# Kernel tuning notes

Measured on AMD Instinct MI355X. Metric: run time of the kernel, lower is better.

Reference implementation:

```python
import jax, jax.numpy as jnp
import numpy as np

S, B, D, H, E, K, DF = 1024, 16, 512, 8, 16, 2, 2048
HD = D // H
EPS = 1e-5


def _layernorm(x, g, b):
    m = x.mean(-1, keepdims=True)
    v = ((x - m) ** 2).mean(-1, keepdims=True)
    return (x - m) / jnp.sqrt(v + EPS) * g + b


def setup_inputs() -> dict:
    key = jax.random.key(0)
    ks = jax.random.split(key, 10)
    s = 0.02
    return {
        "src": jax.random.normal(ks[0], (S, B, D), jnp.float32),
        "pos": jax.random.normal(ks[1], (S, B, D), jnp.float32),
        "in_proj_w": jax.random.normal(ks[2], (3 * D, D), jnp.float32) * s,
        "in_proj_b": jnp.zeros((3 * D,), jnp.float32),
        "out_w": jax.random.normal(ks[3], (D, D), jnp.float32) * s,
        "out_b": jnp.zeros((D,), jnp.float32),
        "norm1_g": jnp.ones((D,), jnp.float32),
        "norm1_b": jnp.zeros((D,), jnp.float32),
        "gate_w": jax.random.normal(ks[4], (E, D), jnp.float32) * s,
        "gate_b": jnp.zeros((E,), jnp.float32),
        "w1": jax.random.normal(ks[5], (E, DF, D), jnp.float32) * s,
        "b1": jnp.zeros((E, DF), jnp.float32),
        "w2": jax.random.normal(ks[6], (E, D, DF), jnp.float32) * s,
        "b2": jnp.zeros((E, D), jnp.float32),
    }


def reference(src, pos, in_proj_w, in_proj_b, out_w, out_b, norm1_g, norm1_b,
              gate_w, gate_b, w1, b1, w2, b2):
    # ---- self attention (torch nn.MultiheadAttention, seq-first) ----
    qk_in = src + pos                      # q = k = src + pos, v = src
    wq, wk, wv = jnp.split(in_proj_w, 3, axis=0)
    bq, bk, bv = jnp.split(in_proj_b, 3, axis=0)
    q = qk_in @ wq.T + bq                  # [S,B,D]
    k = qk_in @ wk.T + bk
    v = src @ wv.T + bv

    def heads(x):                          # [S,B,D] -> [B,H,S,HD]
        return x.reshape(S, B, H, HD).transpose(1, 2, 0, 3)

    qh, kh, vh = heads(q), heads(k), heads(v)
    scores = jnp.einsum('bhqd,bhkd->bhqk', qh * (1.0 / np.sqrt(HD)), kh)
    attn = jax.nn.softmax(scores, axis=-1)
    o = jnp.einsum('bhqk,bhkd->bhqd', attn, vh)
    o = o.transpose(2, 0, 1, 3).reshape(S, B, D) @ out_w.T + out_b

    x = _layernorm(src + o, norm1_g, norm1_b)  # post-norm residual

    # ---- MoE FFN (FMoE NaiveGate, top-k=2, no capacity drop) ----
    t = x.reshape(S * B, D)                # tokens
    logits = t @ gate_w.T + gate_b         # [T,E]
    topv, topi = jax.lax.top_k(logits, K)  # [T,K]
    gate_score = jax.nn.softmax(topv, axis=-1)
    T = S * B
    comb = jnp.zeros((T, E), t.dtype).at[jnp.arange(T)[:, None], topi].add(gate_score)

    def body(acc, packed):
        W1, B1, W2, B2, c = packed         # per-expert weights + combine col [T]
        h = jax.nn.relu(t @ W1.T + B1)     # [T,DF]
        y = h @ W2.T + B2                  # [T,D]
        return acc + c[:, None] * y, None

    acc, _ = jax.lax.scan(body, jnp.zeros_like(t), (w1, b1, w2, b2, comb.T))
    # pre_lnorm=False branch: output = inp + core_out (internal LN unused)
    return x + acc.reshape(S, B, D)
```

## Files before the change

kernel.cpp:

```cpp
#include <hip/hip_runtime.h>
#include <hip/hip_bf16.h>

typedef float f4 __attribute__((ext_vector_type(4)));
typedef float f32x4 __attribute__((ext_vector_type(4)));
typedef short short8 __attribute__((ext_vector_type(8)));
typedef unsigned short u16x4 __attribute__((ext_vector_type(4)));
typedef unsigned short u16x8 __attribute__((ext_vector_type(8)));
typedef unsigned int u32x4 __attribute__((ext_vector_type(4)));
typedef unsigned int u32x8 __attribute__((ext_vector_type(8)));

#define S_LEN 1024
#define BATCH 16
#define DIM   512
#define NH    8
#define HDIM  64
#define NE    16
#define DFF   2048
#define T_TOK 16384
#define CAP   34816
#define BM    128

__device__ __forceinline__ unsigned short f2bf(float f) {
  union { float f; unsigned u; } v; v.f = f;
  unsigned r = v.u + 0x7fffu + ((v.u >> 16) & 1u);
  return (unsigned short)(r >> 16);
}
__device__ __forceinline__ float bf2f(unsigned short h) {
  union { unsigned u; float f; } v; v.u = ((unsigned)h) << 16;
  return v.f;
}

__device__ __forceinline__ void load_lds16(const void* g, void* l) {
  __builtin_amdgcn_global_load_lds(
      (__attribute__((address_space(1))) void*)(void*)g,
      (__attribute__((address_space(3))) void*)l, 16, 0, 0);
}

__device__ __forceinline__ short8 pack_hi8(const unsigned* val) {
  union { unsigned u[4]; short8 s; } t;
#pragma unroll
  for (int i = 0; i < 4; i++)
    t.u[i] = (val[2 * i] >> 16) | (val[2 * i + 1] & 0xFFFF0000u);
  return t.s;
}
__device__ __forceinline__ short8 pack_lo8(const unsigned* val) {
  union { unsigned u[4]; short8 s; } t;
#pragma unroll
  for (int i = 0; i < 4; i++)
    t.u[i] = (val[2 * i] & 0xFFFFu) | (val[2 * i + 1] << 16);
  return t.s;
}

__global__ __launch_bounds__(256) void k_cvt_bf16(const float* __restrict__ in,
                                                  unsigned short* __restrict__ outb,
                                                  size_t n) {
  size_t i = ((size_t)blockIdx.x * 256 + threadIdx.x) * 4;
  size_t stride = (size_t)gridDim.x * 1024;
  for (; i < n; i += stride) {
    f4 v = *(const f4*)&in[i];
    u16x4 o;
    o[0] = f2bf(v[0]); o[1] = f2bf(v[1]); o[2] = f2bf(v[2]); o[3] = f2bf(v[3]);
    *(u16x4*)&outb[i] = o;
  }
}

__global__ __launch_bounds__(256) void k_split_w(const float* __restrict__ in,
                                                 unsigned short* __restrict__ hi,
                                                 unsigned short* __restrict__ lo,
                                                 size_t n) {
  size_t i = ((size_t)blockIdx.x * 256 + threadIdx.x) * 4;
  size_t stride = (size_t)gridDim.x * 1024;
  for (; i < n; i += stride) {
    f4 v = *(const f4*)&in[i];
    u16x4 h, l;
#pragma unroll
    for (int j = 0; j < 4; j++) {
      unsigned short hh = f2bf(v[j]);
      h[j] = hh;
      l[j] = f2bf(v[j] - bf2f(hh));
    }
    *(u16x4*)&hi[i] = h;
    *(u16x4*)&lo[i] = l;
  }
}

__global__ __launch_bounds__(256) void k_init(int* __restrict__ slotTok,
                                              float* __restrict__ slotW,
                                              int* __restrict__ counts) {
  int i = blockIdx.x * 256 + threadIdx.x;
  if (i < CAP) { slotTok[i] = -1; slotW[i] = 0.f; }
  if (i < NE) counts[i] = 0;
}

__global__ __launch_bounds__(256) void k_zero_pad(const int* __restrict__ counts,
                                                  const int* __restrict__ off_pad,
                                                  unsigned short* __restrict__ Xg) {
  const int e = blockIdx.x;
  const int start = off_pad[e] + counts[e];
  const int end = off_pad[e + 1];
  for (int row = start; row < end; row++)
    *(unsigned int*)&Xg[(size_t)row * DIM + threadIdx.x * 2] = 0u;
}

__global__ __launch_bounds__(256, 2) void k_gemm_split(
    const float* __restrict__ A, const float* __restrict__ A2,
    const unsigned short* __restrict__ Wh, const unsigned short* __restrict__ Wl,
    const float* __restrict__ bias, int epi,
    unsigned* __restrict__ p0, unsigned* __restrict__ p1) {
  __shared__ __align__(16) char smem[33792];
  unsigned short* AhL = (unsigned short*)smem;
  unsigned short* AlL = (unsigned short*)(smem + 8192);
  unsigned short* WhL = (unsigned short*)(smem + 16384);
  unsigned short* WlL = (unsigned short*)(smem + 24576);
  unsigned* bounce = (unsigned*)smem;
  const int tid = threadIdx.x, lane = tid & 63, wid = tid >> 6;
  const int wm = wid >> 1, wn = wid & 1;
  const int m0 = blockIdx.x * 128, n0 = blockIdx.y * 128;
  const int row = tid >> 1, half = tid & 1;
  const int xr = (row >> 1) & 3;
  f32x4 acc[4][4] = {};
  f4 ar[4];
#pragma unroll
  for (int j = 0; j < 4; j++) {
    const size_t aoff = (size_t)(m0 + row) * 512 + half * 16 + j * 4;
    ar[j] = *(const f4*)&A[aoff];
    if (A2) { f4 v2 = *(const f4*)&A2[aoff]; ar[j] += v2; }
  }
  for (int k0 = 0; k0 < 512; k0 += 32) {
    __syncthreads();
    u16x8 hi8[2], lo8[2];
#pragma unroll
    for (int j = 0; j < 16; j++) {
      const float x = ar[j >> 2][j & 3];
      const unsigned short h = f2bf(x);
      hi8[j >> 3][j & 7] = h;
      lo8[j >> 3][j & 7] = f2bf(x - bf2f(h));
    }
    const int c0 = half * 2;
    *(u16x8*)&AhL[row * 32 + (((c0 + 0) ^ xr) << 3)] = hi8[0];
    *(u16x8*)&AhL[row * 32 + (((c0 + 1) ^ xr) << 3)] = hi8[1];
    *(u16x8*)&AlL[row * 32 + (((c0 + 0) ^ xr) << 3)] = lo8[0];
    *(u16x8*)&AlL[row * 32 + (((c0 + 1) ^ xr) << 3)] = lo8[1];
#pragma unroll
    for (int i = 0; i < 2; i++) {
      const int rowW = i * 64 + wid * 16 + (lane >> 2);
      const int clog = (lane & 3) ^ ((rowW >> 1) & 3);
      const size_t woff = (size_t)(n0 + rowW) * 512 + k0 + (clog << 3);
      load_lds16(Wh + woff, &WhL[i * 2048 + wid * 512]);
      load_lds16(Wl + woff, &WlL[i * 2048 + wid * 512]);
    }
    __syncthreads();
    if (k0 + 32 < 512) {
#pragma unroll
      for (int j = 0; j < 4; j++) {
        const size_t aoff = (size_t)(m0 + row) * 512 + k0 + 32 + half * 16 + j * 4;
        ar[j] = *(const f4*)&A[aoff];
        if (A2) { f4 v2 = *(const f4*)&A2[aoff]; ar[j] += v2; }
      }
    }
    const int l15 = lane & 15, lk = lane >> 4;
    const int xa = (l15 >> 1) & 3;
    short8 avh[4], avl[4], bvh[4], bvl[4];
#pragma unroll
    for (int mi = 0; mi < 4; mi++) {
      const int mr = wm * 64 + mi * 16 + l15;
      avh[mi] = *(const short8*)&AhL[mr * 32 + ((lk ^ xa) << 3)];
      avl[mi] = *(const short8*)&AlL[mr * 32 + ((lk ^ xa) << 3)];
    }
#pragma unroll
    for (int ni = 0; ni < 4; ni++) {
      const int nr = wn * 64 + ni * 16 + l15;
      bvh[ni] = *(const short8*)&WhL[nr * 32 + ((lk ^ xa) << 3)];
      bvl[ni] = *(const short8*)&WlL[nr * 32 + ((lk ^ xa) << 3)];
    }
#pragma unroll
    for (int mi = 0; mi < 4; mi++) {
#pragma unroll
      for (int ni = 0; ni < 4; ni++) {
        acc[mi][ni] = __builtin_amdgcn_mfma_f32_16x16x32_bf16(avh[mi], bvh[ni], acc[mi][ni], 0, 0, 0);
        acc[mi][ni] = __builtin_amdgcn_mfma_f32_16x16x32_bf16(avh[mi], bvl[ni], acc[mi][ni], 0, 0, 0);
        acc[mi][ni] = __builtin_amdgcn_mfma_f32_16x16x32_bf16(avl[mi], bvh[ni], acc[mi][ni], 0, 0, 0);
      }
    }
  }
  const int l15 = lane & 15, lq = lane >> 4;
  if (epi == 2) {
    float* of = (float*)p0;
#pragma unroll
    for (int mi = 0; mi < 4; mi++) {
      const int rb = m0 + wm * 64 + mi * 16 + (lq << 2);
#pragma unroll
      for (int ni = 0; ni < 4; ni++) {
        const int n = n0 + wn * 64 + ni * 16 + l15;
        const float bn = bias[n];
#pragma unroll
        for (int r = 0; r < 4; r++)
          of[(size_t)(rb + r) * 512 + n] = acc[mi][ni][r] + bn;
      }
    }
  } else if (epi == 0) {
#pragma unroll
    for (int mi = 0; mi < 4; mi++) {
      const int rb = m0 + wm * 64 + mi * 16 + (lq << 2);
#pragma unroll
      for (int ni = 0; ni < 4; ni++) {
        const int n = n0 + wn * 64 + ni * 16 + l15;
        const float bn = bias[n];
#pragma unroll
        for (int r = 0; r < 4; r++) {
          const int m = rb + r;
          const int bidx = m & 15, ss = m >> 4;
          float v = acc[mi][ni][r] + bn;
          unsigned* pl;
          int nn;
          if (n < 512) { v *= 0.125f; pl = p0; nn = n; }
          else { pl = p1; nn = n - 512; }
          const size_t off = ((size_t)(bidx * NH + (nn >> 6)) * S_LEN + ss) * HDIM + (nn & 63);
          const unsigned short hh = f2bf(v);
          pl[off] = ((unsigned)hh << 16) | (unsigned)f2bf(v - bf2f(hh));
        }
      }
    }
  } else {
    const int s_base = m0 >> 4;
    for (int halfn = 0; halfn < 2; halfn++) {
      __syncthreads();
      if (wn == halfn) {
#pragma unroll
        for (int mi = 0; mi < 4; mi++) {
          const int mlb = wm * 64 + mi * 16 + (lq << 2);
#pragma unroll
          for (int ni = 0; ni < 4; ni++) {
            const int n = n0 + wn * 64 + ni * 16 + l15;
            const float bn = bias[n];
            const int nc = ni * 16 + l15;
#pragma unroll
            for (int r = 0; r < 4; r++) {
              const float v = acc[mi][ni][r] + bn;
              const unsigned short hh = f2bf(v);
              bounce[(mlb + r) * 66 + nc] =
                  ((unsigned)hh << 16) | (unsigned)f2bf(v - bf2f(hh));
            }
          }
        }
      }
      __syncthreads();
#pragma unroll
      for (int i = 0; i < 4; i++) {
        const int idx = tid + 256 * i;
        const int nc = idx & 63, bb = idx >> 6;
        const int ng = n0 + halfn * 64 + nc;
        const int hh_ = ng >> 6, dd = ng & 63;
        u32x8 vals;
#pragma unroll
        for (int s = 0; s < 8; s++) vals[s] = bounce[(s * 16 + bb) * 66 + nc];
        *(u32x8*)&p0[((size_t)(bb * NH + hh_) * HDIM + dd) * S_LEN + s_base] = vals;
      }
    }
  }
}

__global__ __launch_bounds__(256, 4) void k_attn(
    const unsigned* __restrict__ Qp, const unsigned* __restrict__ Kp,
    const unsigned* __restrict__ Vp, float* __restrict__ O) {
  const int q0 = blockIdx.x * 64;
  const int bh = blockIdx.y;
  const int b = bh >> 3, h = bh & 7;
  const size_t base = (size_t)bh * (S_LEN * HDIM);
  __shared__ unsigned short KhL[64][72], KlL[64][72];
  __shared__ unsigned short VhL[64][72], VlL[64][72];
  const int tid = threadIdx.x, lane = tid & 63, w = tid >> 6;
  const int l15 = lane & 15, lq = lane >> 4;
  const int srcA = l15 + 16 * ((2 * lq) & 3);
  const int srcB = l15 + 16 * ((2 * lq + 1) & 3);
  const bool selHi = (lane & 32) != 0;
  short8 qh[2], ql[2];
  {
    const size_t qoff = base + (size_t)(q0 + 16 * w + l15) * HDIM + lq * 8;
    u32x8 qv0 = *(const u32x8*)&Qp[qoff];
    u32x8 qv1 = *(const u32x8*)&Qp[qoff + 32];
    qh[0] = pack_hi8((const unsigned*)&qv0); ql[0] = pack_lo8((const unsigned*)&qv0);
    qh[1] = pack_hi8((const unsigned*)&qv1); ql[1] = pack_lo8((const unsigned*)&qv1);
  }
  const int sr = tid >> 2, sq = (tid & 3) * 16;
  u32x4 kr[4], vr[4];
  {
    const size_t ko = base + (size_t)sr * HDIM + sq;
    const size_t vo = base + (size_t)sr * S_LEN + sq;
#pragma unroll
    for (int i = 0; i < 4; i++) {
      kr[i] = *(const u32x4*)&Kp[ko + 4 * i];
      vr[i] = *(const u32x4*)&Vp[vo + 4 * i];
    }
  }
  float m_ = -1e30f, l_ = 0.f;
  f32x4 acc[4] = {};

  for (int kt = 0; kt < 16; kt++) {
    {
      const unsigned* ku = (const unsigned*)kr;
      const unsigned* vu = (const unsigned*)vr;
      *(short8*)&KhL[sr][sq + 0] = pack_hi8(ku);
      *(short8*)&KhL[sr][sq + 8] = pack_hi8(ku + 8);
      *(short8*)&KlL[sr][sq + 0] = pack_lo8(ku);
      *(short8*)&KlL[sr][sq + 8] = pack_lo8(ku + 8);
      *(short8*)&VhL[sr][sq + 0] = pack_hi8(vu);
      *(short8*)&VhL[sr][sq + 8] = pack_hi8(vu + 8);
      *(short8*)&VlL[sr][sq + 0] = pack_lo8(vu);
      *(short8*)&VlL[sr][sq + 8] = pack_lo8(vu + 8);
    }
    __syncthreads();
    if (kt < 15) {
      const int s0n = (kt + 1) * 64;
      const size_t ko = base + (size_t)(s0n + sr) * HDIM + sq;
      const size_t vo = base + (size_t)sr * S_LEN + s0n + sq;
#pragma unroll
      for (int i = 0; i < 4; i++) {
        kr[i] = *(const u32x4*)&Kp[ko + 4 * i];
        vr[i] = *(const u32x4*)&Vp[vo + 4 * i];
      }
    }
    f32x4 sc[4] = {};
#pragma unroll
    for (int c = 0; c < 2; c++) {
      short8 kfh[4], kfl[4];
#pragma unroll
      for (int n = 0; n < 4; n++) {
        kfh[n] = *(const short8*)&KhL[16 * n + l15][c * 32 + lq * 8];
        kfl[n] = *(const short8*)&KlL[16 * n + l15][c * 32 + lq * 8];
      }
#pragma unroll
      for (int n = 0; n < 4; n++) {
        sc[n] = __builtin_amdgcn_mfma_f32_16x16x32_bf16(kfh[n], qh[c], sc[n], 0, 0, 0);
        sc[n] = __builtin_amdgcn_mfma_f32_16x16x32_bf16(kfl[n], qh[c], sc[n], 0, 0, 0);
        sc[n] = __builtin_amdgcn_mfma_f32_16x16x32_bf16(kfh[n], ql[c], sc[n], 0, 0, 0);
      }
    }
    float tm = fmaxf(fmaxf(fmaxf(sc[0][0], sc[0][1]), fmaxf(sc[0][2], sc[0][3])),
                     fmaxf(fmaxf(sc[1][0], sc[1][1]), fmaxf(sc[1][2], sc[1][3])));
    tm = fmaxf(tm, fmaxf(fmaxf(fmaxf(sc[2][0], sc[2][1]), fmaxf(sc[2][2], sc[2][3])),
                         fmaxf(fmaxf(sc[3][0], sc[3][1]), fmaxf(sc[3][2], sc[3][3]))));
    tm = fmaxf(tm, __shfl_xor(tm, 16));
    tm = fmaxf(tm, __shfl_xor(tm, 32));
    const float mn = fmaxf(m_, tm);
    const float esc = __expf(m_ - mn);
    m_ = mn;
    float rs = 0.f;
    unsigned pk[4][4];
#pragma unroll
    for (int n = 0; n < 4; n++) {
#pragma unroll
      for (int r = 0; r < 4; r++) {
        const float p = __expf(sc[n][r] - mn);
        rs += p;
        const unsigned short hh = f2bf(p);
        pk[n][r] = ((unsigned)hh << 16) | (unsigned)f2bf(p - bf2f(hh));
      }
    }
    rs += __shfl_xor(rs, 16);
    rs += __shfl_xor(rs, 32);
    l_ = l_ * esc + rs;
    float escR[4];
#pragma unroll
    for (int r = 0; r < 4; r++) escR[r] = __shfl(esc, 4 * lq + r);
#pragma unroll
    for (int n = 0; n < 4; n++) {
#pragma unroll
      for (int r = 0; r < 4; r++) acc[n][r] *= escR[r];
    }
#pragma unroll
    for (int c = 0; c < 2; c++) {
      unsigned val[8];
#pragma unroll
      for (int j = 0; j < 8; j++) {
        const int src = (j >> 2) ? srcB : srcA;
        const unsigned sA = (unsigned)__shfl((int)pk[2 * c + 0][j & 3], src);
        const unsigned sB = (unsigned)__shfl((int)pk[2 * c + 1][j & 3], src);
        val[j] = selHi ? sB : sA;
      }
      const short8 ph = pack_hi8(val);
      const short8 plo = pack_lo8(val);
      short8 vfh[4], vfl[4];
#pragma unroll
      for (int n = 0; n < 4; n++) {
        vfh[n] = *(const short8*)&VhL[16 * n + l15][c * 32 + lq * 8];
        vfl[n] = *(const short8*)&VlL[16 * n + l15][c * 32 + lq * 8];
      }
#pragma unroll
      for (int n = 0; n < 4; n++) {
        acc[n] = __builtin_amdgcn_mfma_f32_16x16x32_bf16(ph, vfh[n], acc[n], 0, 0, 0);
        acc[n] = __builtin_amdgcn_mfma_f32_16x16x32_bf16(ph, vfl[n], acc[n], 0, 0, 0);
        acc[n] = __builtin_amdgcn_mfma_f32_16x16x32_bf16(plo, vfh[n], acc[n], 0, 0, 0);
      }
    }
    __syncthreads();
  }
  const float inv = 1.f / l_;
  float invR[4];
#pragma unroll
  for (int r = 0; r < 4; r++) invR[r] = __shfl(inv, 4 * lq + r);
#pragma unroll
  for (int r = 0; r < 4; r++) {
    const int srow = q0 + 16 * w + 4 * lq + r;
    float* orow = &O[((size_t)srow * BATCH + b) * DIM + h * HDIM];
#pragma unroll
    for (int n = 0; n < 4; n++) orow[16 * n + l15] = acc[n][r] * invR[r];
  }
}

__global__ __launch_bounds__(256) void k_ln(const float* __restrict__ src,
                                            const float* __restrict__ proj,
                                            const float* __restrict__ g,
                                            const float* __restrict__ bt,
                                            float* __restrict__ xout) {
  const int wid = threadIdx.x >> 6, lane = threadIdx.x & 63;
  const int tok = blockIdx.x * 4 + wid;
  const size_t base = (size_t)tok * DIM + lane * 8;
  f4 a0 = *(const f4*)&src[base],  a1 = *(const f4*)&src[base + 4];
  f4 p0 = *(const f4*)&proj[base], p1 = *(const f4*)&proj[base + 4];
  float x[8];
  x[0] = a0[0] + p0[0]; x[1] = a0[1] + p0[1]; x[2] = a0[2] + p0[2]; x[3] = a0[3] + p0[3];
  x[4] = a1[0] + p1[0]; x[5] = a1[1] + p1[1]; x[6] = a1[2] + p1[2]; x[7] = a1[3] + p1[3];
  float s = 0.f, sq = 0.f;
#pragma unroll
  for (int j = 0; j < 8; j++) { s += x[j]; sq = fmaf(x[j], x[j], sq); }
#pragma unroll
  for (int d = 1; d < 64; d <<= 1) { s += __shfl_xor(s, d); sq += __shfl_xor(sq, d); }
  const float mean = s * (1.f / 512.f);
  const float var = sq * (1.f / 512.f) - mean * mean;
  const float rstd = 1.f / sqrtf(var + 1e-5f);
  const int ci = lane * 8;
  f4 o0v, o1v;
#pragma unroll
  for (int j = 0; j < 4; j++) o0v[j] = (x[j] - mean) * rstd * g[ci + j] + bt[ci + j];
#pragma unroll
  for (int j = 0; j < 4; j++) o1v[j] = (x[4 + j] - mean) * rstd * g[ci + 4 + j] + bt[ci + 4 + j];
  *(f4*)&xout[base] = o0v;
  *(f4*)&xout[base + 4] = o1v;
}

__global__ __launch_bounds__(256) void k_gate(const float* __restrict__ x,
                                              const float* __restrict__ gw,
                                              const float* __restrict__ gb,
                                              int* __restrict__ topi,
                                              float* __restrict__ topw,
                                              int* __restrict__ counts) {
  __shared__ float xs[16 * 520];
  __shared__ int hist[16];
  const int tid = threadIdx.x;
  const int tl = tid >> 4, e = tid & 15;
  if (tid < 16) hist[tid] = 0;
  const float gbe = gb[e];
  const float* wrow = gw + (size_t)e * DIM;
  for (int tile = 0; tile < 4; tile++) {
    const int t0 = blockIdx.x * 64 + tile * 16;
    __syncthreads();
    {
      const int r = tid >> 4, cbase = (tid & 15) * 32;
#pragma unroll
      for (int j = 0; j < 8; j++) {
        const int c = cbase + j * 4;
        const int ch = c >> 2;
        const int pc = ch ^ ((ch >> 3) & 7);
        *(f4*)&xs[r * 520 + pc * 4] = *(const f4*)&x[(size_t)(t0 + r) * DIM + c];
      }
    }
    __syncthreads();
    float d = gbe;
#pragma unroll 8
    for (int c = 0; c < DIM; c += 4) {
      const int ch = c >> 2;
      const int pc = ch ^ ((ch >> 3) & 7);
      f4 xv = *(const f4*)&xs[tl * 520 + pc * 4];
      f4 wv = *(const f4*)&wrow[c];
      d = fmaf(xv[0], wv[0], d); d = fmaf(xv[1], wv[1], d);
      d = fmaf(xv[2], wv[2], d); d = fmaf(xv[3], wv[3], d);
    }
    float v1 = d, v2 = -1e30f;
    int i1 = e, i2 = 1000;
#pragma unroll
    for (int s = 1; s < 16; s <<= 1) {
      const float ov1 = __shfl_xor(v1, s), ov2 = __shfl_xor(v2, s);
      const int oi1 = __shfl_xor(i1, s), oi2 = __shfl_xor(i2, s);
      if (ov1 > v1 || (ov1 == v1 && oi1 < i1)) {
        float nv2; int ni2;
        if (v1 > ov2 || (v1 == ov2 && i1 < oi2)) { nv2 = v1; ni2 = i1; }
        else { nv2 = ov2; ni2 = oi2; }
        v1 = ov1; i1 = oi1; v2 = nv2; i2 = ni2;
      } else if (ov1 > v2 || (ov1 == v2 && oi1 < i2)) {
        v2 = ov1; i2 = oi1;
      }
    }
    if (e == 0) {
      const int t = t0 + tl;
      const float e1 = __expf(v2 - v1);
      const float inv = 1.f / (1.f + e1);
      topi[2 * t] = i1;  topi[2 * t + 1] = i2;
      topw[2 * t] = inv; topw[2 * t + 1] = e1 * inv;
      atomicAdd(&hist[i1], 1);
      atomicAdd(&hist[i2], 1);
    }
  }
  __syncthreads();
  if (tid < 16 && hist[tid] > 0) atomicAdd(&counts[tid], hist[tid]);
}

__global__ void k_offsets(const int* __restrict__ counts,
                          int* __restrict__ off_pad, int* __restrict__ cursor) {
  if (threadIdx.x == 0) {
    int o = 0;
    off_pad[0] = 0;
    for (int e = 0; e < NE; e++) {
      cursor[e] = 0;
      o += ((counts[e] + BM - 1) / BM) * BM;
      off_pad[e + 1] = o;
    }
  }
}

__global__ __launch_bounds__(256) void k_scatter(const float* __restrict__ x,
                                                 const int* __restrict__ topi,
                                                 const float* __restrict__ topw,
                                                 const int* __restrict__ off_pad,
                                                 int* __restrict__ cursor,
                                                 int* __restrict__ slotTok,
                                                 float* __restrict__ slotW,
                                                 unsigned short* __restrict__ Xg) {
  __shared__ int lcnt[16];
  __shared__ int gbase[16];
  __shared__ int posArr[128];
  const int tid = threadIdx.x;
  const int a0 = blockIdx.x * 128;
  if (tid < 16) lcnt[tid] = 0;
  __syncthreads();
  if (tid < 128) {
    const int a = a0 + tid;
    const int e = topi[a];
    const int lrank = atomicAdd(&lcnt[e], 1);
    posArr[tid] = (e << 24) | lrank;
  }
  __syncthreads();
  if (tid < 16) {
    const int c = lcnt[tid];
    gbase[tid] = (c > 0) ? atomicAdd(&cursor[tid], c) : 0;
  }
  __syncthreads();
  if (tid < 128) {
    const int a = a0 + tid;
    const int pk = posArr[tid];
    const int e = pk >> 24, lrank = pk & 0xffffff;
    const int pos = off_pad[e] + gbase[e] + lrank;
    posArr[tid] = pos;
    slotTok[pos] = a >> 1;
    slotW[pos] = topw[a];
  }
  __syncthreads();
  const int w = tid >> 6, lane = tid & 63;
#pragma unroll 4
  for (int i = 0; i < 32; i++) {
    const int idx = w * 32 + i;
    const int pos = posArr[idx];
    const int tok = (a0 + idx) >> 1;
    const size_t sb = (size_t)tok * DIM + lane * 8;
    f4 v0 = *(const f4*)&x[sb], v1 = *(const f4*)&x[sb + 4];
    u16x8 hh;
    hh[0] = f2bf(v0[0]); hh[1] = f2bf(v0[1]); hh[2] = f2bf(v0[2]); hh[3] = f2bf(v0[3]);
    hh[4] = f2bf(v1[0]); hh[5] = f2bf(v1[1]); hh[6] = f2bf(v1[2]); hh[7] = f2bf(v1[3]);
    *(u16x8*)&Xg[(size_t)pos * DIM + lane * 8] = hh;
  }
}

__global__ __launch_bounds__(256) void k_gemm_bf16(
    const unsigned short* __restrict__ A, int lda,
    const unsigned short* __restrict__ Wb, size_t westride, int ldw, int wrow0,
    const float* __restrict__ bias, int bstride, int brow0,
    int K, int epi,
    unsigned short* __restrict__ Hout, int ldh,
    float* __restrict__ dout,
    const int* __restrict__ slotTok, const float* __restrict__ slotW,
    const int* __restrict__ off_pad) {
  int bx = blockIdx.x;
  const int nwg = gridDim.x;
  if ((nwg & 7) == 0) bx = (bx & 7) * (nwg >> 3) + (bx >> 3);
  const int m0 = bx * BM;
  if (m0 >= off_pad[NE]) return;
  int e = 0;
  while (off_pad[e + 1] <= m0) e++;
  const unsigned short* W = Wb + (size_t)e * westride;
  const int n0 = blockIdx.y * 128;
  __shared__ unsigned short Al[128 * 64];
  __shared__ unsigned short Bl[128 * 64];
  const int tid = threadIdx.x, lane = tid & 63, wid = tid >> 6;
  const int wm = wid >> 1, wn = wid & 1;
  f32x4 acc[4][4] = {};
  const int srow = wid * 32 + (lane >> 3);
  const int scol = (((lane & 7) ^ ((lane >> 3) & 7)) << 3);
  for (int k0 = 0; k0 < K; k0 += 64) {
    const unsigned short* ga = A + (size_t)(m0 + srow) * lda + k0 + scol;
    const unsigned short* gw = W + (size_t)(wrow0 + n0 + srow) * ldw + k0 + scol;
#pragma unroll
    for (int i = 0; i < 4; i++) {
      load_lds16(ga + (size_t)i * 8 * lda, &Al[(wid * 32 + i * 8) * 64]);
      load_lds16(gw + (size_t)i * 8 * ldw, &Bl[(wid * 32 + i * 8) * 64]);
    }
    __syncthreads();
#pragma unroll
    for (int kk = 0; kk < 2; kk++) {
      short8 av[4], bv[4];
      const int ckx = (kk * 4 + (lane >> 4)) ^ (lane & 7);
#pragma unroll
      for (int mi = 0; mi < 4; mi++)
        av[mi] = *(const short8*)&Al[(wm * 64 + mi * 16 + (lane & 15)) * 64 + ckx * 8];
#pragma unroll
      for (int ni = 0; ni < 4; ni++)
        bv[ni] = *(const short8*)&Bl[(wn * 64 + ni * 16 + (lane & 15)) * 64 + ckx * 8];
#pragma unroll
      for (int mi = 0; mi < 4; mi++) {
#pragma unroll
        for (int ni = 0; ni < 4; ni++)
          acc[mi][ni] = __builtin_amdgcn_mfma_f32_16x16x32_bf16(av[mi], bv[ni], acc[mi][ni], 0, 0, 0);
      }
    }
    __syncthreads();
  }
#pragma unroll
  for (int mi = 0; mi < 4; mi++) {
    const int rb = m0 + wm * 64 + mi * 16 + ((lane >> 4) << 2);
#pragma unroll
    for (int ni = 0; ni < 4; ni++) {
      const int n = n0 + wn * 64 + ni * 16 + (lane & 15);
      const float bn = bias ? bias[(size_t)e * bstride + brow0 + n] : 0.f;
      if (epi == 0) {
#pragma unroll
        for (int r = 0; r < 4; r++) {
          float v = acc[mi][ni][r] + bn;
          v = fmaxf(v, 0.f);
          Hout[(size_t)(rb + r) * ldh + n] = f2bf(v);
        }
      } else {
#pragma unroll
        for (int r = 0; r < 4; r++) {
          const int tok = slotTok[rb + r];
          if (tok >= 0) {
            const float v = (acc[mi][ni][r] + bn) * slotW[rb + r];
            atomicAdd(&dout[(size_t)tok * DIM + n], v);
          }
        }
      }
    }
  }
}

extern "C" void kernel_launch(void* const* d_in, const int* in_sizes, int n_in,
                              void* d_out, int out_size, void* d_ws, size_t ws_size,
                              hipStream_t stream) {
  const float* src       = (const float*)d_in[0];
  const float* pos       = (const float*)d_in[1];
  const float* in_proj_w = (const float*)d_in[2];
  const float* in_proj_b = (const float*)d_in[3];
  const float* out_w     = (const float*)d_in[4];
  const float* out_b     = (const float*)d_in[5];
  const float* norm1_g   = (const float*)d_in[6];
  const float* norm1_b   = (const float*)d_in[7];
  const float* gate_w    = (const float*)d_in[8];
  const float* gate_b    = (const float*)d_in[9];
  const float* w1        = (const float*)d_in[10];
  const float* b1        = (const float*)d_in[11];
  const float* w2        = (const float*)d_in[12];
  const float* b2        = (const float*)d_in[13];
  float* out = (float*)d_out;
  char* wsb = (char*)d_ws;

  unsigned* Qp = (unsigned*)(wsb + 0);
  unsigned* Kp = (unsigned*)(wsb + 33554432);
  unsigned* Vp = (unsigned*)(wsb + 67108864);
  float* ob = (float*)(wsb + 100663296);
  float* proj = (float*)(wsb + 0);
  unsigned short* w1b = (unsigned short*)(wsb + 0);
  unsigned short* w2b = (unsigned short*)(wsb + 33554432);
  unsigned short* Xg  = (unsigned short*)(wsb + 67108864);
  unsigned short* Hb  = (unsigned short*)(wsb + 102760448);
  unsigned short* wih = (unsigned short*)(wsb + 134217728);
  unsigned short* wil = (unsigned short*)(wsb + 135790592);
  unsigned short* woh = (unsigned short*)(wsb + 137363456);
  unsigned short* wol = (unsigned short*)(wsb + 137887744);
  char* smallb = wsb + 174063616;
  int*   topi    = (int*)  (smallb + 0);
  float* topw    = (float*)(smallb + 131072);
  int*   slotTok = (int*)  (smallb + 262144);
  float* slotW   = (float*)(smallb + 401408);
  int*   counts  = (int*)  (smallb + 540672);
  int*   off_pad = (int*)  (smallb + 540736);
  int*   cursor  = (int*)  (smallb + 540864);

  k_init<<<(CAP + 255) / 256, 256, 0, stream>>>(slotTok, slotW, counts);
  k_split_w<<<768, 256, 0, stream>>>(in_proj_w, wih, wil, (size_t)1536 * 512);
  k_split_w<<<256, 256, 0, stream>>>(out_w, woh, wol, (size_t)512 * 512);
  k_gemm_split<<<dim3(128, 8), 256, 0, stream>>>(src, pos, wih, wil, in_proj_b, 0, Qp, Kp);
  k_gemm_split<<<dim3(128, 4), 256, 0, stream>>>(src, nullptr, wih + (size_t)1024 * 512,
                                                 wil + (size_t)1024 * 512, in_proj_b + 1024,
                                                 1, Vp, nullptr);
  k_attn<<<dim3(16, 128), 256, 0, stream>>>(Qp, Kp, Vp, ob);
  k_cvt_bf16<<<2048, 256, 0, stream>>>(w2, w2b, (size_t)NE * DIM * DFF);
  k_gemm_split<<<dim3(128, 4), 256, 0, stream>>>(ob, nullptr, woh, wol, out_b,
                                                 2, (unsigned*)proj, nullptr);
  k_ln<<<4096, 256, 0, stream>>>(src, proj, norm1_g, norm1_b, out);
  k_cvt_bf16<<<2048, 256, 0, stream>>>(w1, w1b, (size_t)NE * DFF * DIM);
  k_gate<<<T_TOK / 64, 256, 0, stream>>>(out, gate_w, gate_b, topi, topw, counts);
  k_offsets<<<1, 64, 0, stream>>>(counts, off_pad, cursor);
  k_zero_pad<<<NE, 256, 0, stream>>>(counts, off_pad, Xg);
  k_scatter<<<256, 256, 0, stream>>>(out, topi, topw, off_pad, cursor, slotTok, slotW, Xg);
  for (int p = 0; p < 2; ++p) {
    k_gemm_bf16<<<dim3(CAP / BM, 8), 256, 0, stream>>>(
        Xg, DIM, w1b, (size_t)DFF * DIM, DIM, p * 1024,
        b1, DFF, p * 1024, DIM, 0, Hb, 1024,
        nullptr, nullptr, nullptr, off_pad);
    k_gemm_bf16<<<dim3(CAP / BM, 4), 256, 0, stream>>>(
        Hb, 1024, w2b + (size_t)p * 1024, (size_t)DIM * DFF, DFF, 0,
        (p == 0 ? b2 : nullptr), DIM, 0, 1024, 1, nullptr, 0,
        out, slotTok, slotW, off_pad);
  }
}
```

Before: 886.8 us.

## Replace atomic MoE scatter-add with bf16 expert output buffer and gather combine

```diff
diff --git a/kernel.cpp b/kernel.cpp
--- a/kernel.cpp
+++ b/kernel.cpp
@@ -84,12 +84,8 @@
   }
 }
 
-__global__ __launch_bounds__(256) void k_init(int* __restrict__ slotTok,
-                                              float* __restrict__ slotW,
-                                              int* __restrict__ counts) {
-  int i = blockIdx.x * 256 + threadIdx.x;
-  if (i < CAP) { slotTok[i] = -1; slotW[i] = 0.f; }
-  if (i < NE) counts[i] = 0;
+__global__ __launch_bounds__(64) void k_init(int* __restrict__ counts) {
+  if (threadIdx.x < NE) counts[threadIdx.x] = 0;
 }
 
 __global__ __launch_bounds__(256) void k_zero_pad(const int* __restrict__ counts,
@@ -260,10 +256,10 @@
   }
 }
 
-__global__ __launch_bounds__(256, 4) void k_attn(
+__global__ __launch_bounds__(512, 2) void k_attn(
     const unsigned* __restrict__ Qp, const unsigned* __restrict__ Kp,
     const unsigned* __restrict__ Vp, float* __restrict__ O) {
-  const int q0 = blockIdx.x * 64;
+  const int q0 = blockIdx.x * 128;
   const int bh = blockIdx.y;
   const int b = bh >> 3, h = bh & 7;
   const size_t base = (size_t)bh * (S_LEN * HDIM);
@@ -282,16 +278,13 @@
     qh[0] = pack_hi8((const unsigned*)&qv0); ql[0] = pack_lo8((const unsigned*)&qv0);
     qh[1] = pack_hi8((const unsigned*)&qv1); ql[1] = pack_lo8((const unsigned*)&qv1);
   }
-  const int sr = tid >> 2, sq = (tid & 3) * 16;
-  u32x4 kr[4], vr[4];
+  const int sr = tid >> 3, sq8 = (tid & 7) * 8;
+  u32x4 kr[2], vr[2];
   {
-    const size_t ko = base + (size_t)sr * HDIM + sq;
-    const size_t vo = base + (size_t)sr * S_LEN + sq;
-#pragma unroll
-    for (int i = 0; i < 4; i++) {
-      kr[i] = *(const u32x4*)&Kp[ko + 4 * i];
-      vr[i] = *(const u32x4*)&Vp[vo + 4 * i];
-    }
+    const size_t ko = base + (size_t)sr * HDIM + sq8;
+    const size_t vo = base + (size_t)sr * S_LEN + sq8;
+    kr[0] = *(const u32x4*)&Kp[ko]; kr[1] = *(const u32x4*)&Kp[ko + 4];
+    vr[0] = *(const u32x4*)&Vp[vo]; vr[1] = *(const u32x4*)&Vp[vo + 4];
   }
   float m_ = -1e30f, l_ = 0.f;
   f32x4 acc[4] = {};
@@ -300,25 +293,18 @@
     {
       const unsigned* ku = (const unsigned*)kr;
       const unsigned* vu = (const unsigned*)vr;
-      *(short8*)&KhL[sr][sq + 0] = pack_hi8(ku);
-      *(short8*)&KhL[sr][sq + 8] = pack_hi8(ku + 8);
-      *(short8*)&KlL[sr][sq + 0] = pack_lo8(ku);
-      *(short8*)&KlL[sr][sq + 8] = pack_lo8(ku + 8);
-      *(short8*)&VhL[sr][sq + 0] = pack_hi8(vu);
-      *(short8*)&VhL[sr][sq + 8] = pack_hi8(vu + 8);
-      *(short8*)&VlL[sr][sq + 0] = pack_lo8(vu);
-      *(short8*)&VlL[sr][sq + 8] = pack_lo8(vu + 8);
+      *(short8*)&KhL[sr][sq8] = pack_hi8(ku);
+      *(short8*)&KlL[sr][sq8] = pack_lo8(ku);
+      *(short8*)&VhL[sr][sq8] = pack_hi8(vu);
+      *(short8*)&VlL[sr][sq8] = pack_lo8(vu);
     }
     __syncthreads();
     if (kt < 15) {
       const int s0n = (kt + 1) * 64;
-      const size_t ko = base + (size_t)(s0n + sr) * HDIM + sq;
-      const size_t vo = base + (size_t)sr * S_LEN + s0n + sq;
-#pragma unroll
-      for (int i = 0; i < 4; i++) {
-        kr[i] = *(const u32x4*)&Kp[ko + 4 * i];
-        vr[i] = *(const u32x4*)&Vp[vo + 4 * i];
-      }
+      const size_t ko = base + (size_t)(s0n + sr) * HDIM + sq8;
+      const size_t vo = base + (size_t)sr * S_LEN + s0n + sq8;
+      kr[0] = *(const u32x4*)&Kp[ko]; kr[1] = *(const u32x4*)&Kp[ko + 4];
+      vr[0] = *(const u32x4*)&Vp[vo]; vr[1] = *(const u32x4*)&Vp[vo + 4];
     }
     f32x4 sc[4] = {};
 #pragma unroll
@@ -520,11 +506,9 @@
 
 __global__ __launch_bounds__(256) void k_scatter(const float* __restrict__ x,
                                                  const int* __restrict__ topi,
-                                                 const float* __restrict__ topw,
                                                  const int* __restrict__ off_pad,
                                                  int* __restrict__ cursor,
-                                                 int* __restrict__ slotTok,
-                                                 float* __restrict__ slotW,
+                                                 int* __restrict__ tokSlot,
                                                  unsigned short* __restrict__ Xg) {
   __shared__ int lcnt[16];
   __shared__ int gbase[16];
@@ -551,8 +535,7 @@
     const int e = pk >> 24, lrank = pk & 0xffffff;
     const int pos = off_pad[e] + gbase[e] + lrank;
     posArr[tid] = pos;
-    slotTok[pos] = a >> 1;
-    slotW[pos] = topw[a];
+    tokSlot[a] = pos;
   }
   __syncthreads();
   const int w = tid >> 6, lane = tid & 63;
@@ -576,8 +559,6 @@
     const float* __restrict__ bias, int bstride, int brow0,
     int K, int epi,
     unsigned short* __restrict__ Hout, int ldh,
-    float* __restrict__ dout,
-    const int* __restrict__ slotTok, const float* __restrict__ slotW,
     const int* __restrict__ off_pad) {
   int bx = blockIdx.x;
   const int nwg = gridDim.x;
@@ -629,7 +610,7 @@
 #pragma unroll
     for (int ni = 0; ni < 4; ni++) {
       const int n = n0 + wn * 64 + ni * 16 + (lane & 15);
-      const float bn = bias ? bias[(size_t)e * bstride + brow0 + n] : 0.f;
+      const float bn = (epi != 2) ? bias[(size_t)e * bstride + brow0 + n] : 0.f;
       if (epi == 0) {
 #pragma unroll
         for (int r = 0; r < 4; r++) {
@@ -637,18 +618,39 @@
           v = fmaxf(v, 0.f);
           Hout[(size_t)(rb + r) * ldh + n] = f2bf(v);
         }
+      } else if (epi == 1) {
+#pragma unroll
+        for (int r = 0; r < 4; r++)
+          Hout[(size_t)(rb + r) * ldh + n] = f2bf(acc[mi][ni][r] + bn);
       } else {
 #pragma unroll
         for (int r = 0; r < 4; r++) {
-          const int tok = slotTok[rb + r];
-          if (tok >= 0) {
-            const float v = (acc[mi][ni][r] + bn) * slotW[rb + r];
-            atomicAdd(&dout[(size_t)tok * DIM + n], v);
-          }
+          const size_t yo = (size_t)(rb + r) * ldh + n;
+          Hout[yo] = f2bf(acc[mi][ni][r] + bf2f(Hout[yo]));
         }
       }
     }
   }
+}
+
+__global__ __launch_bounds__(256) void k_combine(const unsigned short* __restrict__ Y,
+                                                 const int* __restrict__ tokSlot,
+                                                 const float* __restrict__ topw,
+                                                 float* __restrict__ out) {
+  const int wid = threadIdx.x >> 6, lane = threadIdx.x & 63;
+  const int t = blockIdx.x * 4 + wid;
+  const int pa = tokSlot[2 * t], pb = tokSlot[2 * t + 1];
+  const float wa = topw[2 * t], wb = topw[2 * t + 1];
+  const size_t ob = (size_t)t * DIM + lane * 8;
+  u16x8 ya = *(const u16x8*)&Y[(size_t)pa * DIM + lane * 8];
+  u16x8 yb = *(const u16x8*)&Y[(size_t)pb * DIM + lane * 8];
+  f4 o0 = *(const f4*)&out[ob], o1 = *(const f4*)&out[ob + 4];
+#pragma unroll
+  for (int j = 0; j < 4; j++) o0[j] += wa * bf2f(ya[j]) + wb * bf2f(yb[j]);
+#pragma unroll
+  for (int j = 0; j < 4; j++) o1[j] += wa * bf2f(ya[4 + j]) + wb * bf2f(yb[4 + j]);
+  *(f4*)&out[ob] = o0;
+  *(f4*)&out[ob + 4] = o1;
 }
 
 extern "C" void kernel_launch(void* const* d_in, const int* in_sizes, int n_in,
@@ -680,6 +682,7 @@
   unsigned short* w2b = (unsigned short*)(wsb + 33554432);
   unsigned short* Xg  = (unsigned short*)(wsb + 67108864);
   unsigned short* Hb  = (unsigned short*)(wsb + 102760448);
+  unsigned short* Yb  = (unsigned short*)(wsb + 138412032);
   unsigned short* wih = (unsigned short*)(wsb + 134217728);
   unsigned short* wil = (unsigned short*)(wsb + 135790592);
   unsigned short* woh = (unsigned short*)(wsb + 137363456);
@@ -687,20 +690,19 @@
   char* smallb = wsb + 174063616;
   int*   topi    = (int*)  (smallb + 0);
   float* topw    = (float*)(smallb + 131072);
-  int*   slotTok = (int*)  (smallb + 262144);
-  float* slotW   = (float*)(smallb + 401408);
+  int*   tokSlot = (int*)  (smallb + 262144);
   int*   counts  = (int*)  (smallb + 540672);
   int*   off_pad = (int*)  (smallb + 540736);
   int*   cursor  = (int*)  (smallb + 540864);
 
-  k_init<<<(CAP + 255) / 256, 256, 0, stream>>>(slotTok, slotW, counts);
+  k_init<<<1, 64, 0, stream>>>(counts);
   k_split_w<<<768, 256, 0, stream>>>(in_proj_w, wih, wil, (size_t)1536 * 512);
   k_split_w<<<256, 256, 0, stream>>>(out_w, woh, wol, (size_t)512 * 512);
   k_gemm_split<<<dim3(128, 8), 256, 0, stream>>>(src, pos, wih, wil, in_proj_b, 0, Qp, Kp);
   k_gemm_split<<<dim3(128, 4), 256, 0, stream>>>(src, nullptr, wih + (size_t)1024 * 512,
                                                  wil + (size_t)1024 * 512, in_proj_b + 1024,
                                                  1, Vp, nullptr);
-  k_attn<<<dim3(16, 128), 256, 0, stream>>>(Qp, Kp, Vp, ob);
+  k_attn<<<dim3(8, 128), 512, 0, stream>>>(Qp, Kp, Vp, ob);
   k_cvt_bf16<<<2048, 256, 0, stream>>>(w2, w2b, (size_t)NE * DIM * DFF);
   k_gemm_split<<<dim3(128, 4), 256, 0, stream>>>(ob, nullptr, woh, wol, out_b,
                                                  2, (unsigned*)proj, nullptr);
@@ -709,15 +711,14 @@
   k_gate<<<T_TOK / 64, 256, 0, stream>>>(out, gate_w, gate_b, topi, topw, counts);
   k_offsets<<<1, 64, 0, stream>>>(counts, off_pad, cursor);
   k_zero_pad<<<NE, 256, 0, stream>>>(counts, off_pad, Xg);
-  k_scatter<<<256, 256, 0, stream>>>(out, topi, topw, off_pad, cursor, slotTok, slotW, Xg);
-  for (int p = 0; p < 2; ++p) {
-    k_gemm_bf16<<<dim3(CAP / BM, 8), 256, 0, stream>>>(
-        Xg, DIM, w1b, (size_t)DFF * DIM, DIM, p * 1024,
-        b1, DFF, p * 1024, DIM, 0, Hb, 1024,
-        nullptr, nullptr, nullptr, off_pad);
+  k_scatter<<<256, 256, 0, stream>>>(out, topi, off_pad, cursor, tokSlot, Xg);
+  for (int p = 0; p < 4; ++p) {
     k_gemm_bf16<<<dim3(CAP / BM, 4), 256, 0, stream>>>(
-        Hb, 1024, w2b + (size_t)p * 1024, (size_t)DIM * DFF, DFF, 0,
-        (p == 0 ? b2 : nullptr), DIM, 0, 1024, 1, nullptr, 0,
-        out, slotTok, slotW, off_pad);
-  }
-}
+        Xg, DIM, w1b, (size_t)DFF * DIM, DIM, p * 512,
+        b1, DFF, p * 512, DIM, 0, Hb, 512, off_pad);
+    k_gemm_bf16<<<dim3(CAP / BM, 4), 256, 0, stream>>>(
+        Hb, 512, w2b + (size_t)p * 512, (size_t)DIM * DFF, DFF, 0,
+        b2, DIM, 0, 512, (p == 0 ? 1 : 2), Yb, DIM, off_pad);
+  }
+  k_combine<<<T_TOK / 4, 256, 0, stream>>>(Yb, tokSlot, topw, out);
+}
```

Result: no change. 892.0 us (+0.6%).
